# Optimization experiments

Measured on AMD Instinct MI355X. Metric: run time of the kernel, lower is better.

The kernel has to match this reference:

```python
import jax, jax.numpy as jnp
import numpy as np

T, B, I, H = 512, 256, 128, 256

def setup_inputs() -> dict:
    key = jax.random.key(0)
    ks = jax.random.split(key, 8)
    s_ih = 1.0 / np.sqrt(H)
    return {
        "x": jax.random.normal(ks[0], (T, B, I), dtype=jnp.float32),
        "gt": jax.random.uniform(ks[1], (T, B, 1), dtype=jnp.float32),
        "W_ih": jax.random.uniform(ks[2], (3 * H, I), minval=-s_ih, maxval=s_ih, dtype=jnp.float32),
        "W_hh": jax.random.uniform(ks[3], (3 * H, H), minval=-s_ih, maxval=s_ih, dtype=jnp.float32),
        "b_ih": jax.random.uniform(ks[4], (3 * H,), minval=-s_ih, maxval=s_ih, dtype=jnp.float32),
        "b_hh": jax.random.uniform(ks[5], (3 * H,), minval=-s_ih, maxval=s_ih, dtype=jnp.float32),
        "W_dec": jax.random.uniform(ks[6], (1, H), minval=-s_ih, maxval=s_ih, dtype=jnp.float32),
        "b_dec": jax.random.uniform(ks[7], (1,), minval=-s_ih, maxval=s_ih, dtype=jnp.float32),
    }

def reference(x, gt, W_ih, W_hh, b_ih, b_hh, W_dec, b_dec):
    h_dim = W_hh.shape[1]

    def step(h, inp):
        xt, gtt = inp  # xt: [B, I], gtt: [B, 1]
        gi = xt @ W_ih.T + b_ih          # [B, 3H]
        gh = h @ W_hh.T + b_hh           # [B, 3H]
        i_r, i_z, i_n = jnp.split(gi, 3, axis=-1)
        h_r, h_z, h_n = jnp.split(gh, 3, axis=-1)
        r = jax.nn.sigmoid(i_r + h_r)
        z = jax.nn.sigmoid(i_z + h_z)
        n = jnp.tanh(i_n + r * h_n)
        h_new = (1.0 - z) * n + z * h    # [B, H]
        logit = h_new @ W_dec.T + b_dec  # [B, 1]
        # BCE(sigmoid(logit), gt), reduction='sum': stable log-sigmoid form
        loss = -jnp.sum(gtt * jax.nn.log_sigmoid(logit)
                        + (1.0 - gtt) * jax.nn.log_sigmoid(-logit))
        return h_new, loss

    h0 = jnp.zeros((x.shape[1], h_dim), dtype=x.dtype)
    _, losses = jax.lax.scan(step, h0, (x[:-1], gt[1:]))
    return jnp.sum(losses)
```

## Files before the change

### kernel.cpp

```cpp
#include <hip/hip_runtime.h>
#include <hip/hip_bf16.h>


typedef __bf16 bf16x8_t __attribute__((ext_vector_type(8)));
typedef float floatx4_t __attribute__((ext_vector_type(4)));
typedef int intx4_t __attribute__((ext_vector_type(4)));
typedef unsigned int u32;
typedef u32 u32x4_t __attribute__((ext_vector_type(4)));

#define SW 2032.0f
#define SH 127.0f
#define INV_S (1.0f / (127.0f * 2032.0f))
#define NL2E (-1.44269504088896f)
#define CRZ (NL2E * INV_S)
#define CN (2.0f * NL2E * INV_S)

static __device__ inline u32 pack2bf(float a, float b) {
  __bf16 x = (__bf16)a, y = (__bf16)b;
  unsigned short ux = *(unsigned short*)&x, uy = *(unsigned short*)&y;
  return (u32)ux | ((u32)uy << 16);
}

__global__ void prep_kernel(const float* __restrict__ Whh,
                            const float* __restrict__ Wdec,
                            const float* __restrict__ Wih,
                            char* __restrict__ Wq, char* __restrict__ wdq,
                            __bf16* __restrict__ Wihb,
                            float* __restrict__ h_ws, float* __restrict__ out) {
  int idx = blockIdx.x * 256 + threadIdx.x;
  for (int i = idx; i < 768 * 256; i += 65536) {
    int v = (int)rintf(Whh[i] * SW);
    v = v > 127 ? 127 : (v < -127 ? -127 : v);
    Wq[i] = (char)v;
  }
  for (int i = idx; i < 768 * 128; i += 65536) Wihb[i] = (__bf16)Wih[i];
  if (idx < 256) {
    int v = (int)rintf(Wdec[idx] * SW);
    v = v > 127 ? 127 : (v < -127 ? -127 : v);
    wdq[idx] = (char)v;
  }
  if (idx < 65536) h_ws[idx] = 0.f;
  if (idx == 0) out[0] = 0.f;
}

__global__ __launch_bounds__(256) void xconv_kernel(const float* __restrict__ x,
                                                    __bf16* __restrict__ xb) {
  const size_t i = ((size_t)blockIdx.x * 256 + threadIdx.x) * 8;
  floatx4_t a = *(const floatx4_t*)(x + i);
  floatx4_t b = *(const floatx4_t*)(x + i + 4);
  bf16x8_t t;
#pragma unroll
  for (int j = 0; j < 4; ++j) {
    t[j] = (__bf16)a[j];
    t[4 + j] = (__bf16)b[j];
  }
  *(bf16x8_t*)(xb + i) = t;
}

__global__ __launch_bounds__(256) void gemm1_kernel(
    const __bf16* __restrict__ xb,
    const __bf16* __restrict__ Wihb,
    const float* __restrict__ bih, const float* __restrict__ bhh,
    u32* __restrict__ giw) {
  __shared__ __bf16 As[128][144];
  __shared__ __bf16 Bs[128][144];

  const int tid = threadIdx.x;
  const int w = tid >> 6, lane = tid & 63;
  const int q = lane >> 4, nh = lane & 15;
  const int n0 = blockIdx.x * 128;
  const int b0 = blockIdx.y * 128;
  const int wm = w >> 1, wn = w & 1;

  {
    const bf16x8_t* sa = (const bf16x8_t*)(Wihb + (size_t)n0 * 128);
    const bf16x8_t* sb = (const bf16x8_t*)(xb + (size_t)b0 * 128);
    const int rr = tid >> 4, cc = (tid & 15) * 8;
#pragma unroll
    for (int v = 0; v < 8; ++v) {
      *(bf16x8_t*)&As[v * 16 + rr][cc] = sa[v * 256 + tid];
      *(bf16x8_t*)&Bs[v * 16 + rr][cc] = sb[v * 256 + tid];
    }
  }
  __syncthreads();

  floatx4_t acc[4][4];
#pragma unroll
  for (int a = 0; a < 4; ++a)
#pragma unroll
    for (int b = 0; b < 4; ++b)
#pragma unroll
      for (int j = 0; j < 4; ++j) acc[a][b][j] = 0.f;

#pragma unroll
  for (int kk = 0; kk < 4; ++kk) {
    bf16x8_t af[4], bf[4];
#pragma unroll
    for (int mt = 0; mt < 4; ++mt)
      af[mt] = *(const bf16x8_t*)&As[wm * 64 + mt * 16 + nh][kk * 32 + q * 8];
#pragma unroll
    for (int nt = 0; nt < 4; ++nt)
      bf[nt] = *(const bf16x8_t*)&Bs[wn * 64 + nt * 16 + nh][kk * 32 + q * 8];
#pragma unroll
    for (int mt = 0; mt < 4; ++mt)
#pragma unroll
      for (int nt = 0; nt < 4; ++nt)
        acc[mt][nt] = __builtin_amdgcn_mfma_f32_16x16x32_bf16(
            af[mt], bf[nt], acc[mt][nt], 0, 0, 0);
  }

  const int gate = n0 >> 8;
  const float sc = (gate < 2) ? NL2E : (2.0f * NL2E);
  const int wr_base = ((n0 & 255) >> 5) + wm * 2;
#pragma unroll
  for (int a = 0; a < 2; ++a) {
    const int nnA = n0 + wm * 64 + a * 32 + q * 4;
    floatx4_t biasA = *(const floatx4_t*)(bih + nnA);
    floatx4_t biasB = *(const floatx4_t*)(bih + nnA + 16);
    if (gate < 2) {
      floatx4_t c1 = *(const floatx4_t*)(bhh + nnA);
      floatx4_t c2 = *(const floatx4_t*)(bhh + nnA + 16);
#pragma unroll
      for (int j = 0; j < 4; ++j) {
        biasA[j] += c1[j];
        biasB[j] += c2[j];
      }
    }
    const int wrec = wr_base + a;
#pragma unroll
    for (int nt = 0; nt < 4; ++nt) {
      const int bb = b0 + wn * 64 + nt * 16 + nh;
      const int tl = bb >> 8, gg = (bb >> 2) & 63, jb = bb & 3;
      size_t U =
          (((size_t)tl * 64 + gg) * 3 + gate) * 512 + wrec * 64 + jb * 16 + q * 4;
      u32x4_t pv;
#pragma unroll
      for (int j = 0; j < 4; ++j)
        pv[j] = pack2bf((acc[2 * a][nt][j] + biasA[j]) * sc,
                        (acc[2 * a + 1][nt][j] + biasB[j]) * sc);
      *(u32x4_t*)(giw + U) = pv;
    }
  }
}

__global__ __launch_bounds__(1024) void rec_kernel(
    const char* __restrict__ Wq,
    const char* __restrict__ wdq,
    const u32* __restrict__ gi,
    const float* __restrict__ gt, const float* __restrict__ bdec,
    const float* __restrict__ bhh, float* __restrict__ h_ws,
    float* __restrict__ out, int t0, int tc) {
  __shared__ char hb[2][4][288];
  __shared__ float lp[4][2048];

  const int tid = threadIdx.x;
  const int w = tid >> 6, lane = tid & 63;
  const int q = lane >> 4, nh = lane & 15;
  const int g = blockIdx.x;
  const int col = w * 16 + nh;
  const int wp = w >> 1;
  const int hi = w & 1;

  intx4_t wf[3][4];
#pragma unroll
  for (int c = 0; c < 3; ++c) {
    const int n = c * 256 + col;
#pragma unroll
    for (int kb = 0; kb < 4; ++kb)
      wf[c][kb] = *(const intx4_t*)(Wq + (size_t)n * 256 + kb * 64 + q * 16);
  }
  intx4_t wdfk;
  {
    const int kb = (w >= 12) ? (w - 12) : 0;
    intx4_t z = {0, 0, 0, 0};
    intx4_t v = *(const intx4_t*)(wdq + kb * 64 + q * 16);
    wdfk = (nh == 0) ? v : z;
  }

  const float bn2 = 2.0f * NL2E * bhh[512 + col];
  const float bdec0 = bdec[0];

  if (tid < 256) {
    const int rr = tid >> 6, c0 = (tid & 63) * 4;
    u32 p = 0;
#pragma unroll
    for (int j = 0; j < 4; ++j) {
      int a = (int)rintf(h_ws[(size_t)(g * 4 + rr) * 256 + c0 + j] * SH);
      a = a > 127 ? 127 : (a < -127 ? -127 : a);
      p |= ((u32)(a & 255)) << (8 * j);
    }
    *(u32*)&hb[0][rr][c0] = p;
  }
  float ho = h_ws[(size_t)(g * 4 + q) * 256 + col];
  __syncthreads();

  const int tcm1 = tc - 1;
  const size_t boff = (size_t)wp * 64 + q * 16 + nh;
  u32 GA[3], GB[3];
  {
    size_t u0 = ((size_t)g * 3) * 512 + boff;
#pragma unroll
    for (int c = 0; c < 3; ++c) GA[c] = gi[u0 + c * 512];
    const int t1s = tc > 1 ? 1 : 0;
    size_t u1 = (((size_t)t1s * 64 + g) * 3) * 512 + boff;
#pragma unroll
    for (int c = 0; c < 3; ++c) GB[c] = gi[u1 + c * 512];
  }

  auto STEP = [&](int T, u32* G, int TPRE) {
    const int pb = T & 1;
    intx4_t hbf[4];
#pragma unroll
    for (int kb = 0; kb < 4; ++kb)
      hbf[kb] = *(const intx4_t*)&hb[pb][nh >> 2][kb * 64 + q * 16];

    float gv0, gv1, gv2;
    if (hi) {
      gv0 = __uint_as_float(G[0] & 0xffff0000u);
      gv1 = __uint_as_float(G[1] & 0xffff0000u);
      gv2 = __uint_as_float(G[2] & 0xffff0000u);
    } else {
      gv0 = __uint_as_float(G[0] << 16);
      gv1 = __uint_as_float(G[1] << 16);
      gv2 = __uint_as_float(G[2] << 16);
    }
    {
      size_t up = (((size_t)TPRE * 64 + g) * 3) * 512 + boff;
#pragma unroll
      for (int c = 0; c < 3; ++c) G[c] = gi[up + c * 512];
    }

    intx4_t acc[3];
#pragma unroll
    for (int cs = 0; cs < 3; ++cs)
#pragma unroll
      for (int jj = 0; jj < 4; ++jj) acc[cs][jj] = 0;

#pragma unroll
    for (int kb = 0; kb < 4; ++kb)
#pragma unroll
      for (int cs = 0; cs < 3; ++cs)
        acc[cs] = __builtin_amdgcn_mfma_i32_16x16x64_i8(hbf[kb], wf[cs][kb],
                                                        acc[cs], 0, 0, 0);

    if (w >= 12) {
      intx4_t hsel = (w == 12) ? hbf[0]
                   : (w == 13) ? hbf[1]
                   : (w == 14) ? hbf[2] : hbf[3];
      intx4_t facc = {0, 0, 0, 0};
      facc = __builtin_amdgcn_mfma_i32_16x16x64_i8(hsel, wdfk, facc, 0, 0, 0);
      if (nh == 0 && T >= 1) lp[w - 12][(T - 1) * 4 + q] = (float)facc[0];
    }

    float rr0 = __builtin_amdgcn_rcpf(
        1.f + __builtin_amdgcn_exp2f((float)acc[0][0] * CRZ + gv0));
    float zz0 = __builtin_amdgcn_rcpf(
        1.f + __builtin_amdgcn_exp2f((float)acc[1][0] * CRZ + gv1));
    float hn2 = (float)acc[2][0] * CN + bn2;
    float tv0 = 2.f * __builtin_amdgcn_rcpf(
                          1.f + __builtin_amdgcn_exp2f(rr0 * hn2 + gv2)) -
                1.f;
    float hnew = tv0 + zz0 * (ho - tv0);
    ho = hnew;
    int h8 = (int)rintf(hnew * SH);
    hb[1 - pb][q][col] = (char)h8;

    asm volatile("s_waitcnt lgkmcnt(0)" ::: "memory");
    __builtin_amdgcn_s_barrier();
    asm volatile("" ::: "memory");
  };

  int t = 0;
#pragma unroll 1
  for (; t + 1 < tc; t += 2) {
    STEP(t, GA, (t + 2 <= tcm1) ? t + 2 : tcm1);
    STEP(t + 1, GB, (t + 3 <= tcm1) ? t + 3 : tcm1);
  }
  if (t < tc) STEP(t, GA, tcm1);

  if (w >= 12) {
    const int kb = w - 12;
    intx4_t b = *(const intx4_t*)&hb[tc & 1][nh >> 2][kb * 64 + q * 16];
    intx4_t fac2 = {0, 0, 0, 0};
    fac2 = __builtin_amdgcn_mfma_i32_16x16x64_i8(b, wdfk, fac2, 0, 0, 0);
    if (nh == 0) lp[kb][(tc - 1) * 4 + q] = (float)fac2[0];
  }
  __syncthreads();

  float loss = 0.f;
  for (int i = tid; i < tc * 4; i += 1024) {
    float l = (lp[0][i] + lp[1][i] + lp[2][i] + lp[3][i]) * INV_S + bdec0;
    float gtv = gt[(size_t)(t0 + (i >> 2) + 1) * 256 + g * 4 + (i & 3)];
    float t1 = log1pf(__expf(-fabsf(l)));
    loss += gtv * (fmaxf(-l, 0.f) + t1) + (1.f - gtv) * (fmaxf(l, 0.f) + t1);
  }
  loss += __shfl_xor(loss, 1);
  loss += __shfl_xor(loss, 2);
  loss += __shfl_xor(loss, 4);
  loss += __shfl_xor(loss, 8);
  loss += __shfl_xor(loss, 16);
  loss += __shfl_xor(loss, 32);
  if (lane == 0) atomicAdd(out, loss);

  h_ws[(size_t)(g * 4 + q) * 256 + col] = ho;
}

extern "C" void kernel_launch(void* const* d_in, const int* in_sizes, int n_in,
                              void* d_out, int out_size, void* d_ws,
                              size_t ws_size, hipStream_t stream) {
  const float* x = (const float*)d_in[0];
  const float* gt = (const float*)d_in[1];
  const float* Wih = (const float*)d_in[2];
  const float* Whh = (const float*)d_in[3];
  const float* bih = (const float*)d_in[4];
  const float* bhh = (const float*)d_in[5];
  const float* Wdec = (const float*)d_in[6];
  const float* bdec = (const float*)d_in[7];
  float* out = (float*)d_out;

  char* ws = (char*)d_ws;
  char* Wq = ws;
  char* wdq = ws + 196608;
  float* h_ws = (float*)(ws + 197120);
  __bf16* Wihb = (__bf16*)(ws + 459264);
  char* dyn = ws + 655872;
  const size_t per_step = (size_t)393216 + 65536;
  size_t avail = ws_size > 655872 ? ws_size - 655872 : per_step;
  int Tc = (int)(avail / per_step);
  if (Tc < 1) Tc = 1;
  if (Tc > 511) Tc = 511;
  __bf16* xb = (__bf16*)dyn;
  u32* gi = (u32*)(dyn + (size_t)Tc * 65536);

  prep_kernel<<<256, 256, 0, stream>>>(Whh, Wdec, Wih, Wq, wdq, Wihb, h_ws,
                                       out);
  for (int t0 = 0; t0 < 511; t0 += Tc) {
    const int tc = (511 - t0 < Tc) ? (511 - t0) : Tc;
    xconv_kernel<<<tc * 16, 256, 0, stream>>>(x + (size_t)t0 * 256 * 128, xb);
    gemm1_kernel<<<dim3(6, tc * 2), 256, 0, stream>>>(xb, Wihb, bih, bhh, gi);
    rec_kernel<<<64, 1024, 0, stream>>>(Wq, wdq, gi, gt, bdec, bhh, h_ws, out,
                                        t0, tc);
  }
}
```

Baseline: 518.0 us.

## Fuse input projection GEMM into recurrent kernel in 16-step chunks

Removes the separate x-to-bf16 conversion and input-projection GEMM kernels. The recurrent kernel now computes, for each 16-timestep chunk, its own block's input-gate projections into shared memory before running the sequential steps. The loss is accumulated per chunk instead of at the end. This avoids writing and rereading the large gate-projection buffer through global memory, and avoids the extra launches. In exchange, the GEMM work now runs inside only 64 blocks and is serialized with the recurrence, with extra barriers per chunk.

```diff
diff --git a/kernel.cpp b/kernel.cpp
--- a/kernel.cpp
+++ b/kernel.cpp
@@ -14,6 +14,7 @@
 #define NL2E (-1.44269504088896f)
 #define CRZ (NL2E * INV_S)
 #define CN (2.0f * NL2E * INV_S)
+#define CH 16
 
 static __device__ inline u32 pack2bf(float a, float b) {
   __bf16 x = (__bf16)a, y = (__bf16)b;
@@ -26,7 +27,7 @@
                             const float* __restrict__ Wih,
                             char* __restrict__ Wq, char* __restrict__ wdq,
                             __bf16* __restrict__ Wihb,
-                            float* __restrict__ h_ws, float* __restrict__ out) {
+                            float* __restrict__ out) {
   int idx = blockIdx.x * 256 + threadIdx.x;
   for (int i = idx; i < 768 * 256; i += 65536) {
     int v = (int)rintf(Whh[i] * SW);
@@ -39,119 +40,23 @@
     v = v > 127 ? 127 : (v < -127 ? -127 : v);
     wdq[idx] = (char)v;
   }
-  if (idx < 65536) h_ws[idx] = 0.f;
   if (idx == 0) out[0] = 0.f;
 }
 
-__global__ __launch_bounds__(256) void xconv_kernel(const float* __restrict__ x,
-                                                    __bf16* __restrict__ xb) {
-  const size_t i = ((size_t)blockIdx.x * 256 + threadIdx.x) * 8;
-  floatx4_t a = *(const floatx4_t*)(x + i);
-  floatx4_t b = *(const floatx4_t*)(x + i + 4);
-  bf16x8_t t;
-#pragma unroll
-  for (int j = 0; j < 4; ++j) {
-    t[j] = (__bf16)a[j];
-    t[4 + j] = (__bf16)b[j];
-  }
-  *(bf16x8_t*)(xb + i) = t;
-}
-
-__global__ __launch_bounds__(256) void gemm1_kernel(
-    const __bf16* __restrict__ xb,
-    const __bf16* __restrict__ Wihb,
-    const float* __restrict__ bih, const float* __restrict__ bhh,
-    u32* __restrict__ giw) {
-  __shared__ __bf16 As[128][144];
-  __shared__ __bf16 Bs[128][144];
-
-  const int tid = threadIdx.x;
-  const int w = tid >> 6, lane = tid & 63;
-  const int q = lane >> 4, nh = lane & 15;
-  const int n0 = blockIdx.x * 128;
-  const int b0 = blockIdx.y * 128;
-  const int wm = w >> 1, wn = w & 1;
-
-  {
-    const bf16x8_t* sa = (const bf16x8_t*)(Wihb + (size_t)n0 * 128);
-    const bf16x8_t* sb = (const bf16x8_t*)(xb + (size_t)b0 * 128);
-    const int rr = tid >> 4, cc = (tid & 15) * 8;
-#pragma unroll
-    for (int v = 0; v < 8; ++v) {
-      *(bf16x8_t*)&As[v * 16 + rr][cc] = sa[v * 256 + tid];
-      *(bf16x8_t*)&Bs[v * 16 + rr][cc] = sb[v * 256 + tid];
-    }
-  }
-  __syncthreads();
-
-  floatx4_t acc[4][4];
-#pragma unroll
-  for (int a = 0; a < 4; ++a)
-#pragma unroll
-    for (int b = 0; b < 4; ++b)
-#pragma unroll
-      for (int j = 0; j < 4; ++j) acc[a][b][j] = 0.f;
-
-#pragma unroll
-  for (int kk = 0; kk < 4; ++kk) {
-    bf16x8_t af[4], bf[4];
-#pragma unroll
-    for (int mt = 0; mt < 4; ++mt)
-      af[mt] = *(const bf16x8_t*)&As[wm * 64 + mt * 16 + nh][kk * 32 + q * 8];
-#pragma unroll
-    for (int nt = 0; nt < 4; ++nt)
-      bf[nt] = *(const bf16x8_t*)&Bs[wn * 64 + nt * 16 + nh][kk * 32 + q * 8];
-#pragma unroll
-    for (int mt = 0; mt < 4; ++mt)
-#pragma unroll
-      for (int nt = 0; nt < 4; ++nt)
-        acc[mt][nt] = __builtin_amdgcn_mfma_f32_16x16x32_bf16(
-            af[mt], bf[nt], acc[mt][nt], 0, 0, 0);
-  }
-
-  const int gate = n0 >> 8;
-  const float sc = (gate < 2) ? NL2E : (2.0f * NL2E);
-  const int wr_base = ((n0 & 255) >> 5) + wm * 2;
-#pragma unroll
-  for (int a = 0; a < 2; ++a) {
-    const int nnA = n0 + wm * 64 + a * 32 + q * 4;
-    floatx4_t biasA = *(const floatx4_t*)(bih + nnA);
-    floatx4_t biasB = *(const floatx4_t*)(bih + nnA + 16);
-    if (gate < 2) {
-      floatx4_t c1 = *(const floatx4_t*)(bhh + nnA);
-      floatx4_t c2 = *(const floatx4_t*)(bhh + nnA + 16);
-#pragma unroll
-      for (int j = 0; j < 4; ++j) {
-        biasA[j] += c1[j];
-        biasB[j] += c2[j];
-      }
-    }
-    const int wrec = wr_base + a;
-#pragma unroll
-    for (int nt = 0; nt < 4; ++nt) {
-      const int bb = b0 + wn * 64 + nt * 16 + nh;
-      const int tl = bb >> 8, gg = (bb >> 2) & 63, jb = bb & 3;
-      size_t U =
-          (((size_t)tl * 64 + gg) * 3 + gate) * 512 + wrec * 64 + jb * 16 + q * 4;
-      u32x4_t pv;
-#pragma unroll
-      for (int j = 0; j < 4; ++j)
-        pv[j] = pack2bf((acc[2 * a][nt][j] + biasA[j]) * sc,
-                        (acc[2 * a + 1][nt][j] + biasB[j]) * sc);
-      *(u32x4_t*)(giw + U) = pv;
-    }
-  }
-}
-
-__global__ __launch_bounds__(1024) void rec_kernel(
+__global__ __launch_bounds__(1024) void rec2_kernel(
     const char* __restrict__ Wq,
     const char* __restrict__ wdq,
-    const u32* __restrict__ gi,
-    const float* __restrict__ gt, const float* __restrict__ bdec,
-    const float* __restrict__ bhh, float* __restrict__ h_ws,
-    float* __restrict__ out, int t0, int tc) {
+    const float* __restrict__ x,
+    const float* __restrict__ gt,
+    const float* __restrict__ bdec, const float* __restrict__ bhh,
+    const float* __restrict__ bih,
+    const __bf16* __restrict__ Wihb,
+    float* __restrict__ out) {
+  __shared__ u32 gi_s[CH][3][512];
+  __shared__ __bf16 xs[64][136];
+  __shared__ __bf16 wsb[128][136];
   __shared__ char hb[2][4][288];
-  __shared__ float lp[4][2048];
+  __shared__ float lp[4][64];
 
   const int tid = threadIdx.x;
   const int w = tid >> 6, lane = tid & 63;
@@ -160,6 +65,7 @@
   const int col = w * 16 + nh;
   const int wp = w >> 1;
   const int hi = w & 1;
+  const int boff = wp * 64 + q * 16 + nh;
 
   intx4_t wf[3][4];
 #pragma unroll
@@ -180,129 +86,182 @@
   const float bn2 = 2.0f * NL2E * bhh[512 + col];
   const float bdec0 = bdec[0];
 
-  if (tid < 256) {
-    const int rr = tid >> 6, c0 = (tid & 63) * 4;
-    u32 p = 0;
-#pragma unroll
-    for (int j = 0; j < 4; ++j) {
-      int a = (int)rintf(h_ws[(size_t)(g * 4 + rr) * 256 + c0 + j] * SH);
-      a = a > 127 ? 127 : (a < -127 ? -127 : a);
-      p |= ((u32)(a & 255)) << (8 * j);
-    }
-    *(u32*)&hb[0][rr][c0] = p;
-  }
-  float ho = h_ws[(size_t)(g * 4 + q) * 256 + col];
-  __syncthreads();
-
-  const int tcm1 = tc - 1;
-  const size_t boff = (size_t)wp * 64 + q * 16 + nh;
-  u32 GA[3], GB[3];
-  {
-    size_t u0 = ((size_t)g * 3) * 512 + boff;
-#pragma unroll
-    for (int c = 0; c < 3; ++c) GA[c] = gi[u0 + c * 512];
-    const int t1s = tc > 1 ? 1 : 0;
-    size_t u1 = (((size_t)t1s * 64 + g) * 3) * 512 + boff;
-#pragma unroll
-    for (int c = 0; c < 3; ++c) GB[c] = gi[u1 + c * 512];
-  }
-
-  auto STEP = [&](int T, u32* G, int TPRE) {
-    const int pb = T & 1;
-    intx4_t hbf[4];
-#pragma unroll
-    for (int kb = 0; kb < 4; ++kb)
-      hbf[kb] = *(const intx4_t*)&hb[pb][nh >> 2][kb * 64 + q * 16];
-
-    float gv0, gv1, gv2;
-    if (hi) {
-      gv0 = __uint_as_float(G[0] & 0xffff0000u);
-      gv1 = __uint_as_float(G[1] & 0xffff0000u);
-      gv2 = __uint_as_float(G[2] & 0xffff0000u);
-    } else {
-      gv0 = __uint_as_float(G[0] << 16);
-      gv1 = __uint_as_float(G[1] << 16);
-      gv2 = __uint_as_float(G[2] << 16);
-    }
+  for (int i2 = tid; i2 < 576; i2 += 1024) ((u32*)hb)[i2] = 0;
+  float ho = 0.f;
+  float loss = 0.f;
+
+  const int wpair = w & 3;
+  const int btile = w >> 2;
+
+#pragma unroll 1
+  for (int c = 0; c < 32; ++c) {
+    const int t0c = c * CH;
+
     {
-      size_t up = (((size_t)TPRE * 64 + g) * 3) * 512 + boff;
-#pragma unroll
-      for (int c = 0; c < 3; ++c) G[c] = gi[up + c * 512];
-    }
-
-    intx4_t acc[3];
-#pragma unroll
-    for (int cs = 0; cs < 3; ++cs)
-#pragma unroll
-      for (int jj = 0; jj < 4; ++jj) acc[cs][jj] = 0;
-
-#pragma unroll
-    for (int kb = 0; kb < 4; ++kb)
+      const int row = tid >> 4, cc = (tid & 15) * 8;
+      const size_t gx =
+          ((size_t)(t0c + (row >> 2)) * 256 + g * 4 + (row & 3)) * 128 + cc;
+      floatx4_t a = *(const floatx4_t*)(x + gx);
+      floatx4_t b = *(const floatx4_t*)(x + gx + 4);
+      bf16x8_t tv;
+#pragma unroll
+      for (int j = 0; j < 4; ++j) {
+        tv[j] = (__bf16)a[j];
+        tv[4 + j] = (__bf16)b[j];
+      }
+      *(bf16x8_t*)&xs[row][cc] = tv;
+    }
+
+#pragma unroll 1
+    for (int s = 0; s < 6; ++s) {
+      __syncthreads();
+      {
+        const int row = tid >> 3, cc = (tid & 7) * 16;
+        const __bf16* src = Wihb + (size_t)(s * 128 + row) * 128 + cc;
+        *(bf16x8_t*)&wsb[row][cc] = *(const bf16x8_t*)src;
+        *(bf16x8_t*)&wsb[row][cc + 8] = *(const bf16x8_t*)(src + 8);
+      }
+      __syncthreads();
+
+      floatx4_t a0, a1;
+#pragma unroll
+      for (int j = 0; j < 4; ++j) {
+        a0[j] = 0.f;
+        a1[j] = 0.f;
+      }
+#pragma unroll
+      for (int kk = 0; kk < 4; ++kk) {
+        bf16x8_t A0 = *(const bf16x8_t*)&wsb[wpair * 32 + nh][kk * 32 + q * 8];
+        bf16x8_t A1 =
+            *(const bf16x8_t*)&wsb[wpair * 32 + 16 + nh][kk * 32 + q * 8];
+        bf16x8_t B = *(const bf16x8_t*)&xs[btile * 16 + nh][kk * 32 + q * 8];
+        a0 = __builtin_amdgcn_mfma_f32_16x16x32_bf16(A0, B, a0, 0, 0, 0);
+        a1 = __builtin_amdgcn_mfma_f32_16x16x32_bf16(A1, B, a1, 0, 0, 0);
+      }
+
+      const int gate = s >> 1;
+      const float sc = (gate < 2) ? NL2E : (2.0f * NL2E);
+      const int n0 = s * 128 + wpair * 32 + q * 4;
+      floatx4_t biasA = *(const floatx4_t*)(bih + n0);
+      floatx4_t biasB = *(const floatx4_t*)(bih + n0 + 16);
+      if (gate < 2) {
+        floatx4_t c1 = *(const floatx4_t*)(bhh + n0);
+        floatx4_t c2 = *(const floatx4_t*)(bhh + n0 + 16);
+#pragma unroll
+        for (int j = 0; j < 4; ++j) {
+          biasA[j] += c1[j];
+          biasB[j] += c2[j];
+        }
+      }
+      const int wrec = (s & 1) * 4 + wpair;
+      const int b = btile * 16 + nh, tl2 = b >> 2, jb = b & 3;
+      u32x4_t pv;
+#pragma unroll
+      for (int j = 0; j < 4; ++j)
+        pv[j] = pack2bf((a0[j] + biasA[j]) * sc, (a1[j] + biasB[j]) * sc);
+      *(u32x4_t*)&gi_s[tl2][gate][wrec * 64 + jb * 16 + q * 4] = pv;
+    }
+    __syncthreads();
+
+    const int te = (c == 31) ? 15 : 16;
+#pragma unroll 1
+    for (int tl = 0; tl < te; ++tl) {
+      const int t = t0c + tl;
+      const int pb = t & 1;
+      intx4_t hbf[4];
+#pragma unroll
+      for (int kb = 0; kb < 4; ++kb)
+        hbf[kb] = *(const intx4_t*)&hb[pb][nh >> 2][kb * 64 + q * 16];
+
+      const u32 G0 = gi_s[tl][0][boff];
+      const u32 G1 = gi_s[tl][1][boff];
+      const u32 G2 = gi_s[tl][2][boff];
+      float gv0, gv1, gv2;
+      if (hi) {
+        gv0 = __uint_as_float(G0 & 0xffff0000u);
+        gv1 = __uint_as_float(G1 & 0xffff0000u);
+        gv2 = __uint_as_float(G2 & 0xffff0000u);
+      } else {
+        gv0 = __uint_as_float(G0 << 16);
+        gv1 = __uint_as_float(G1 << 16);
+        gv2 = __uint_as_float(G2 << 16);
+      }
+
+      intx4_t acc[3];
 #pragma unroll
       for (int cs = 0; cs < 3; ++cs)
-        acc[cs] = __builtin_amdgcn_mfma_i32_16x16x64_i8(hbf[kb], wf[cs][kb],
-                                                        acc[cs], 0, 0, 0);
-
-    if (w >= 12) {
-      intx4_t hsel = (w == 12) ? hbf[0]
-                   : (w == 13) ? hbf[1]
-                   : (w == 14) ? hbf[2] : hbf[3];
-      intx4_t facc = {0, 0, 0, 0};
-      facc = __builtin_amdgcn_mfma_i32_16x16x64_i8(hsel, wdfk, facc, 0, 0, 0);
-      if (nh == 0 && T >= 1) lp[w - 12][(T - 1) * 4 + q] = (float)facc[0];
-    }
-
-    float rr0 = __builtin_amdgcn_rcpf(
-        1.f + __builtin_amdgcn_exp2f((float)acc[0][0] * CRZ + gv0));
-    float zz0 = __builtin_amdgcn_rcpf(
-        1.f + __builtin_amdgcn_exp2f((float)acc[1][0] * CRZ + gv1));
-    float hn2 = (float)acc[2][0] * CN + bn2;
-    float tv0 = 2.f * __builtin_amdgcn_rcpf(
-                          1.f + __builtin_amdgcn_exp2f(rr0 * hn2 + gv2)) -
-                1.f;
-    float hnew = tv0 + zz0 * (ho - tv0);
-    ho = hnew;
-    int h8 = (int)rintf(hnew * SH);
-    hb[1 - pb][q][col] = (char)h8;
-
-    asm volatile("s_waitcnt lgkmcnt(0)" ::: "memory");
-    __builtin_amdgcn_s_barrier();
-    asm volatile("" ::: "memory");
-  };
-
-  int t = 0;
-#pragma unroll 1
-  for (; t + 1 < tc; t += 2) {
-    STEP(t, GA, (t + 2 <= tcm1) ? t + 2 : tcm1);
-    STEP(t + 1, GB, (t + 3 <= tcm1) ? t + 3 : tcm1);
-  }
-  if (t < tc) STEP(t, GA, tcm1);
-
-  if (w >= 12) {
-    const int kb = w - 12;
-    intx4_t b = *(const intx4_t*)&hb[tc & 1][nh >> 2][kb * 64 + q * 16];
-    intx4_t fac2 = {0, 0, 0, 0};
-    fac2 = __builtin_amdgcn_mfma_i32_16x16x64_i8(b, wdfk, fac2, 0, 0, 0);
-    if (nh == 0) lp[kb][(tc - 1) * 4 + q] = (float)fac2[0];
-  }
-  __syncthreads();
-
-  float loss = 0.f;
-  for (int i = tid; i < tc * 4; i += 1024) {
-    float l = (lp[0][i] + lp[1][i] + lp[2][i] + lp[3][i]) * INV_S + bdec0;
-    float gtv = gt[(size_t)(t0 + (i >> 2) + 1) * 256 + g * 4 + (i & 3)];
-    float t1 = log1pf(__expf(-fabsf(l)));
-    loss += gtv * (fmaxf(-l, 0.f) + t1) + (1.f - gtv) * (fmaxf(l, 0.f) + t1);
-  }
-  loss += __shfl_xor(loss, 1);
-  loss += __shfl_xor(loss, 2);
-  loss += __shfl_xor(loss, 4);
-  loss += __shfl_xor(loss, 8);
-  loss += __shfl_xor(loss, 16);
-  loss += __shfl_xor(loss, 32);
-  if (lane == 0) atomicAdd(out, loss);
-
-  h_ws[(size_t)(g * 4 + q) * 256 + col] = ho;
+#pragma unroll
+        for (int jj = 0; jj < 4; ++jj) acc[cs][jj] = 0;
+
+#pragma unroll
+      for (int kb = 0; kb < 4; ++kb)
+#pragma unroll
+        for (int cs = 0; cs < 3; ++cs)
+          acc[cs] = __builtin_amdgcn_mfma_i32_16x16x64_i8(hbf[kb], wf[cs][kb],
+                                                          acc[cs], 0, 0, 0);
+
+      if (w >= 12) {
+        intx4_t hsel = (w == 12)   ? hbf[0]
+                       : (w == 13) ? hbf[1]
+                       : (w == 14) ? hbf[2]
+                                   : hbf[3];
+        intx4_t facc = {0, 0, 0, 0};
+        facc =
+            __builtin_amdgcn_mfma_i32_16x16x64_i8(hsel, wdfk, facc, 0, 0, 0);
+        if (nh == 0 && t >= 1) lp[w - 12][tl * 4 + q] = (float)facc[0];
+      }
+
+      float rr0 = __builtin_amdgcn_rcpf(
+          1.f + __builtin_amdgcn_exp2f((float)acc[0][0] * CRZ + gv0));
+      float zz0 = __builtin_amdgcn_rcpf(
+          1.f + __builtin_amdgcn_exp2f((float)acc[1][0] * CRZ + gv1));
+      float hn2 = (float)acc[2][0] * CN + bn2;
+      float tv0 = 2.f * __builtin_amdgcn_rcpf(
+                            1.f + __builtin_amdgcn_exp2f(rr0 * hn2 + gv2)) -
+                  1.f;
+      float hnew = tv0 + zz0 * (ho - tv0);
+      ho = hnew;
+      int h8 = (int)rintf(hnew * SH);
+      hb[1 - pb][q][col] = (char)h8;
+
+      asm volatile("s_waitcnt lgkmcnt(0)" ::: "memory");
+      __builtin_amdgcn_s_barrier();
+      asm volatile("" ::: "memory");
+    }
+
+    if (c == 31 && w >= 12) {
+      const int kb = w - 12;
+      intx4_t b2 = *(const intx4_t*)&hb[1][nh >> 2][kb * 64 + q * 16];
+      intx4_t f2 = {0, 0, 0, 0};
+      f2 = __builtin_amdgcn_mfma_i32_16x16x64_i8(b2, wdfk, f2, 0, 0, 0);
+      if (nh == 0) lp[kb][15 * 4 + q] = (float)f2[0];
+    }
+    __syncthreads();
+
+    if (tid < 64) {
+      const int slot = tid >> 2;
+      const int gidx = t0c + slot - 1;
+      if (gidx >= 0 && gidx <= 510) {
+        float l =
+            (lp[0][tid] + lp[1][tid] + lp[2][tid] + lp[3][tid]) * INV_S +
+            bdec0;
+        float gtv = gt[(size_t)(gidx + 1) * 256 + g * 4 + (tid & 3)];
+        float t1 = log1pf(__expf(-fabsf(l)));
+        loss +=
+            gtv * (fmaxf(-l, 0.f) + t1) + (1.f - gtv) * (fmaxf(l, 0.f) + t1);
+      }
+    }
+  }
+
+  if (w == 0) {
+    loss += __shfl_xor(loss, 1);
+    loss += __shfl_xor(loss, 2);
+    loss += __shfl_xor(loss, 4);
+    loss += __shfl_xor(loss, 8);
+    loss += __shfl_xor(loss, 16);
+    loss += __shfl_xor(loss, 32);
+    if (lane == 0) atomicAdd(out, loss);
+  }
 }
 
 extern "C" void kernel_launch(void* const* d_in, const int* in_sizes, int n_in,
@@ -321,24 +280,9 @@
   char* ws = (char*)d_ws;
   char* Wq = ws;
   char* wdq = ws + 196608;
-  float* h_ws = (float*)(ws + 197120);
-  __bf16* Wihb = (__bf16*)(ws + 459264);
-  char* dyn = ws + 655872;
-  const size_t per_step = (size_t)393216 + 65536;
-  size_t avail = ws_size > 655872 ? ws_size - 655872 : per_step;
-  int Tc = (int)(avail / per_step);
-  if (Tc < 1) Tc = 1;
-  if (Tc > 511) Tc = 511;
-  __bf16* xb = (__bf16*)dyn;
-  u32* gi = (u32*)(dyn + (size_t)Tc * 65536);
-
-  prep_kernel<<<256, 256, 0, stream>>>(Whh, Wdec, Wih, Wq, wdq, Wihb, h_ws,
+  __bf16* Wihb = (__bf16*)(ws + 197120);
+
+  prep_kernel<<<256, 256, 0, stream>>>(Whh, Wdec, Wih, Wq, wdq, Wihb, out);
+  rec2_kernel<<<64, 1024, 0, stream>>>(Wq, wdq, x, gt, bdec, bhh, bih, Wihb,
                                        out);
-  for (int t0 = 0; t0 < 511; t0 += Tc) {
-    const int tc = (511 - t0 < Tc) ? (511 - t0) : Tc;
-    xconv_kernel<<<tc * 16, 256, 0, stream>>>(x + (size_t)t0 * 256 * 128, xb);
-    gemm1_kernel<<<dim3(6, tc * 2), 256, 0, stream>>>(xb, Wihb, bih, bhh, gi);
-    rec_kernel<<<64, 1024, 0, stream>>>(Wq, wdq, gi, gt, bdec, bhh, h_ws, out,
-                                        t0, tc);
-  }
-}
+}
```

Result: slower. 742.9 us (+43.4%).

## Keep W_ih fragments in registers and loop each block over eight batch tiles

Applied to the files above, without the earlier changes.

The input-projection GEMM now loads its W_ih A-fragments into registers once per block and reuses them across up to eight consecutive 128-row batch tiles, reading x fragments straight from global memory instead of staging both operands in LDS. This removes the LDS staging, the barrier and the redundant W_ih reloads per tile, and cuts the grid size by a factor of eight. The cost is higher register pressure, uncoalesced-looking direct global loads for B fragments, and less parallelism per launch. The recurrent kernel, which likely dominates, is unchanged.

```diff
diff --git a/kernel.cpp b/kernel.cpp
--- a/kernel.cpp
+++ b/kernel.cpp
@@ -57,88 +57,96 @@
   *(bf16x8_t*)(xb + i) = t;
 }
 
-__global__ __launch_bounds__(256) void gemm1_kernel(
+__global__ __launch_bounds__(256, 2) void gemm2_kernel(
     const __bf16* __restrict__ xb,
     const __bf16* __restrict__ Wihb,
     const float* __restrict__ bih, const float* __restrict__ bhh,
-    u32* __restrict__ giw) {
-  __shared__ __bf16 As[128][144];
-  __shared__ __bf16 Bs[128][144];
-
+    u32* __restrict__ giw, int tc) {
   const int tid = threadIdx.x;
   const int w = tid >> 6, lane = tid & 63;
   const int q = lane >> 4, nh = lane & 15;
   const int n0 = blockIdx.x * 128;
-  const int b0 = blockIdx.y * 128;
   const int wm = w >> 1, wn = w & 1;
 
-  {
-    const bf16x8_t* sa = (const bf16x8_t*)(Wihb + (size_t)n0 * 128);
-    const bf16x8_t* sb = (const bf16x8_t*)(xb + (size_t)b0 * 128);
-    const int rr = tid >> 4, cc = (tid & 15) * 8;
-#pragma unroll
-    for (int v = 0; v < 8; ++v) {
-      *(bf16x8_t*)&As[v * 16 + rr][cc] = sa[v * 256 + tid];
-      *(bf16x8_t*)&Bs[v * 16 + rr][cc] = sb[v * 256 + tid];
-    }
-  }
-  __syncthreads();
-
-  floatx4_t acc[4][4];
-#pragma unroll
-  for (int a = 0; a < 4; ++a)
-#pragma unroll
-    for (int b = 0; b < 4; ++b)
-#pragma unroll
-      for (int j = 0; j < 4; ++j) acc[a][b][j] = 0.f;
-
-#pragma unroll
-  for (int kk = 0; kk < 4; ++kk) {
-    bf16x8_t af[4], bf[4];
-#pragma unroll
-    for (int mt = 0; mt < 4; ++mt)
-      af[mt] = *(const bf16x8_t*)&As[wm * 64 + mt * 16 + nh][kk * 32 + q * 8];
-#pragma unroll
-    for (int nt = 0; nt < 4; ++nt)
-      bf[nt] = *(const bf16x8_t*)&Bs[wn * 64 + nt * 16 + nh][kk * 32 + q * 8];
-#pragma unroll
-    for (int mt = 0; mt < 4; ++mt)
-#pragma unroll
-      for (int nt = 0; nt < 4; ++nt)
-        acc[mt][nt] = __builtin_amdgcn_mfma_f32_16x16x32_bf16(
-            af[mt], bf[nt], acc[mt][nt], 0, 0, 0);
-  }
+  bf16x8_t af[4][4];
+#pragma unroll
+  for (int mt = 0; mt < 4; ++mt)
+#pragma unroll
+    for (int kk = 0; kk < 4; ++kk)
+      af[mt][kk] = *(const bf16x8_t*)(Wihb +
+                                      (size_t)(n0 + wm * 64 + mt * 16 + nh) *
+                                          128 +
+                                      kk * 32 + q * 8);
 
   const int gate = n0 >> 8;
   const float sc = (gate < 2) ? NL2E : (2.0f * NL2E);
   const int wr_base = ((n0 & 255) >> 5) + wm * 2;
+  floatx4_t biasA[2], biasB[2];
 #pragma unroll
   for (int a = 0; a < 2; ++a) {
     const int nnA = n0 + wm * 64 + a * 32 + q * 4;
-    floatx4_t biasA = *(const floatx4_t*)(bih + nnA);
-    floatx4_t biasB = *(const floatx4_t*)(bih + nnA + 16);
+    biasA[a] = *(const floatx4_t*)(bih + nnA);
+    biasB[a] = *(const floatx4_t*)(bih + nnA + 16);
     if (gate < 2) {
       floatx4_t c1 = *(const floatx4_t*)(bhh + nnA);
       floatx4_t c2 = *(const floatx4_t*)(bhh + nnA + 16);
 #pragma unroll
       for (int j = 0; j < 4; ++j) {
-        biasA[j] += c1[j];
-        biasB[j] += c2[j];
+        biasA[a][j] += c1[j];
+        biasB[a][j] += c2[j];
       }
     }
-    const int wrec = wr_base + a;
-#pragma unroll
-    for (int nt = 0; nt < 4; ++nt) {
-      const int bb = b0 + wn * 64 + nt * 16 + nh;
-      const int tl = bb >> 8, gg = (bb >> 2) & 63, jb = bb & 3;
-      size_t U =
-          (((size_t)tl * 64 + gg) * 3 + gate) * 512 + wrec * 64 + jb * 16 + q * 4;
-      u32x4_t pv;
-#pragma unroll
-      for (int j = 0; j < 4; ++j)
-        pv[j] = pack2bf((acc[2 * a][nt][j] + biasA[j]) * sc,
-                        (acc[2 * a + 1][nt][j] + biasB[j]) * sc);
-      *(u32x4_t*)(giw + U) = pv;
+  }
+
+  const int ntiles = tc * 2;
+#pragma unroll 1
+  for (int it = 0; it < 8; ++it) {
+    const int bt = blockIdx.y * 8 + it;
+    if (bt >= ntiles) break;
+    const int ts = bt >> 1, b0 = (bt & 1) * 128;
+
+    floatx4_t acc[4][4];
+#pragma unroll
+    for (int a = 0; a < 4; ++a)
+#pragma unroll
+      for (int b = 0; b < 4; ++b)
+#pragma unroll
+        for (int j = 0; j < 4; ++j) acc[a][b][j] = 0.f;
+
+#pragma unroll
+    for (int kk = 0; kk < 4; ++kk) {
+      bf16x8_t bf[4];
+#pragma unroll
+      for (int nt = 0; nt < 4; ++nt)
+        bf[nt] = *(const bf16x8_t*)(xb +
+                                    (size_t)(ts * 256 + b0 + wn * 64 +
+                                             nt * 16 + nh) *
+                                        128 +
+                                    kk * 32 + q * 8);
+#pragma unroll
+      for (int mt = 0; mt < 4; ++mt)
+#pragma unroll
+        for (int nt = 0; nt < 4; ++nt)
+          acc[mt][nt] = __builtin_amdgcn_mfma_f32_16x16x32_bf16(
+              af[mt][kk], bf[nt], acc[mt][nt], 0, 0, 0);
+    }
+
+#pragma unroll
+    for (int a = 0; a < 2; ++a) {
+      const int wrec = wr_base + a;
+#pragma unroll
+      for (int nt = 0; nt < 4; ++nt) {
+        const int bb = b0 + wn * 64 + nt * 16 + nh;
+        const int gg = bb >> 2, jb = bb & 3;
+        size_t U = (((size_t)ts * 64 + gg) * 3 + gate) * 512 + wrec * 64 +
+                   jb * 16 + q * 4;
+        u32x4_t pv;
+#pragma unroll
+        for (int j = 0; j < 4; ++j)
+          pv[j] = pack2bf((acc[2 * a][nt][j] + biasA[a][j]) * sc,
+                          (acc[2 * a + 1][nt][j] + biasB[a][j]) * sc);
+        *(u32x4_t*)(giw + U) = pv;
+      }
     }
   }
 }
@@ -337,7 +345,8 @@
   for (int t0 = 0; t0 < 511; t0 += Tc) {
     const int tc = (511 - t0 < Tc) ? (511 - t0) : Tc;
     xconv_kernel<<<tc * 16, 256, 0, stream>>>(x + (size_t)t0 * 256 * 128, xb);
-    gemm1_kernel<<<dim3(6, tc * 2), 256, 0, stream>>>(xb, Wihb, bih, bhh, gi);
+    gemm2_kernel<<<dim3(6, (tc * 2 + 7) / 8), 256, 0, stream>>>(xb, Wihb, bih,
+                                                                bhh, gi, tc);
     rec_kernel<<<64, 1024, 0, stream>>>(Wq, wdq, gi, gt, bdec, bhh, h_ws, out,
                                         t0, tc);
   }
```

Result: no change. 523.7 us (+1.1%).
